# Kernel tuning notes

Hardware: AMD Instinct MI355X
Metric: run time of the kernel (lower is better)

The kernel has to match this reference:

```python
import jax, jax.numpy as jnp
import numpy as np

NPOINT = 2048
RADII = (0.4, 0.8)
NSAMPLES = (16, 32)
EPS = 1e-5


def _fps(xyz, npoint):
    # iterative farthest point sampling, start at index 0 (matches CUDA kernel)
    B, N, _ = xyz.shape

    def step(carry, _):
        dist, last = carry  # dist [B,N], last [B]
        lx = jnp.take_along_axis(xyz, last[:, None, None], axis=1)  # [B,1,3]
        d = jnp.sum((xyz - lx) ** 2, axis=-1)  # [B,N]
        dist = jnp.minimum(dist, d)
        nxt = jnp.argmax(dist, axis=1).astype(jnp.int32)
        return (dist, nxt), last

    init = (jnp.full((B, N), 1e10, xyz.dtype), jnp.zeros((B,), jnp.int32))
    _, idxs = jax.lax.scan(step, init, None, length=npoint)
    return idxs.T  # [B, npoint]


def _ball_query(radius, nsample, xyz, new_xyz):
    # first-nsample points within radius, in original order; pad with first hit (0 if none)
    N = xyz.shape[1]
    d2 = jnp.sum((new_xyz[:, :, None, :] - xyz[:, None, :, :]) ** 2, axis=-1)  # [B,S,N]
    mask = d2 < radius * radius
    ar = jnp.arange(N, dtype=jnp.int32)
    key = jnp.where(mask, ar, N + ar)  # in-range first, stable original order
    order = jnp.argsort(key, axis=-1)[..., :nsample].astype(jnp.int32)  # [B,S,ns]
    cnt = mask.sum(axis=-1, keepdims=True)  # [B,S,1]
    valid = jnp.arange(nsample) < cnt
    return jnp.where(valid, order, order[..., :1])


def _bn_relu(x):
    # training-mode BatchNorm (gamma=1, beta=0) over all dims but channel (last)
    red = tuple(range(x.ndim - 1))
    mu = x.mean(axis=red, keepdims=True)
    var = x.var(axis=red, keepdims=True)
    return jax.nn.relu((x - mu) * jax.lax.rsqrt(var + EPS))


def _scale(xyz, new_xyz, feats, radius, nsample, ws):
    idx = _ball_query(radius, nsample, xyz, new_xyz)  # [B,S,ns]
    B, S, ns = idx.shape
    flat = idx.reshape(B, S * ns)
    gx = jnp.take_along_axis(xyz, flat[..., None], axis=1).reshape(B, S, ns, 3)
    gx = gx - new_xyz[:, :, None, :]  # relative coords
    gf = jnp.take_along_axis(feats, flat[..., None], axis=1).reshape(B, S, ns, -1)
    h = jnp.concatenate([gx, gf], axis=-1)  # [B,S,ns,3+C]
    for w in ws:
        h = _bn_relu(h @ w)  # pointwise conv (kernel 1) + BN + ReLU
    return h.max(axis=2)  # max-pool over group -> [B,S,Cout]


def setup_inputs() -> dict:
    key = jax.random.key(0)
    ks = jax.random.split(key, 16)
    s = 0.02
    return {
        "xyz": jax.random.normal(ks[0], (8, 8192, 3), jnp.float32),
        "features": jax.random.normal(ks[1], (8, 8192, 64), jnp.float32),
        "w0_0": jax.random.normal(ks[2], (67, 64), jnp.float32) * s,
        "w0_1": jax.random.normal(ks[3], (64, 64), jnp.float32) * s,
        "w0_2": jax.random.normal(ks[4], (64, 128), jnp.float32) * s,
        "w1_0": jax.random.normal(ks[5], (67, 64), jnp.float32) * s,
        "w1_1": jax.random.normal(ks[6], (64, 64), jnp.float32) * s,
        "w1_2": jax.random.normal(ks[7], (64, 128), jnp.float32) * s,
        "agg_w": jax.random.normal(ks[8], (256, 256), jnp.float32) * s,
        "agg_b": jax.random.normal(ks[9], (256,), jnp.float32) * s,
        "conf_w": jax.random.normal(ks[10], (256, 256), jnp.float32) * s,
        "cls_w": jax.random.normal(ks[11], (256, 3), jnp.float32) * s,
        "cls_b": jax.random.normal(ks[12], (3,), jnp.float32) * s,
    }


def reference(xyz, features, w0_0, w0_1, w0_2, w1_0, w1_1, w1_2,
              agg_w, agg_b, conf_w, cls_w, cls_b):
    idx = _fps(xyz, NPOINT)  # [B,S]
    new_xyz = jnp.take_along_axis(xyz, idx[..., None], axis=1)  # [B,S,3]
    f0 = _scale(xyz, new_xyz, features, RADII[0], NSAMPLES[0], (w0_0, w0_1, w0_2))
    f1 = _scale(xyz, new_xyz, features, RADII[1], NSAMPLES[1], (w1_0, w1_1, w1_2))
    h = jnp.concatenate([f0, f1], axis=-1)  # [B,S,256]
    h = _bn_relu(h @ agg_w + agg_b)  # aggregation Linear + BN + ReLU
    c = _bn_relu(h @ conf_w)  # confidence hidden layer
    cls = c @ cls_w + cls_b  # [B,S,num_class]
    return new_xyz, h, cls
```

## Files before the change

### kernel.cpp

```cpp
#include <hip/hip_runtime.h>
#include <cstdint>
#include <cstddef>

constexpr int Bb = 8;
constexpr int Nn = 8192;
constexpr int Ss = 2048;
constexpr int BS = Bb * Ss;
constexpr int NSL = 32;

typedef float vfloat2 __attribute__((ext_vector_type(2)));

__global__ __launch_bounds__(1024) void fps_kernel(const float* __restrict__ xyz,
                                                   float* __restrict__ new_xyz) {
  __shared__ float lx[Nn * 3];
  __shared__ int sidx[Ss];
  __shared__ unsigned long long slotV[2];
  __shared__ int slotI[2];
  const int b = blockIdx.x;
  const int tid = threadIdx.x;
  const float* xb = xyz + (size_t)b * Nn * 3;
  for (int e = tid; e < Nn * 3; e += 1024) lx[e] = xb[e];
  if (tid == 0) {
    slotV[0] = 0ull; slotV[1] = 0ull;
    slotI[0] = 0x7fffffff; slotI[1] = 0x7fffffff;
  }
  __syncthreads();

  vfloat2 px2[4], py2[4], pz2[4], df2[4];
  double dist[8];
#pragma unroll
  for (int jj = 0; jj < 4; ++jj) {
    const int p0 = tid + (2 * jj) * 1024, p1 = tid + (2 * jj + 1) * 1024;
    px2[jj] = (vfloat2){lx[p0 * 3 + 0], lx[p1 * 3 + 0]};
    py2[jj] = (vfloat2){lx[p0 * 3 + 1], lx[p1 * 3 + 1]};
    pz2[jj] = (vfloat2){lx[p0 * 3 + 2], lx[p1 * 3 + 2]};
    df2[jj] = (vfloat2){3.0e38f, 3.0e38f};
    dist[2 * jj] = 1e10;
    dist[2 * jj + 1] = 1e10;
  }
  float lmax = 3.0e38f;
  int cur = 0;
  double lv = -1.0;
  int li = 0x7fffffff;
  float lv32 = -1.0f;
  float wv32_c = -1.0f;
  for (int i = 0; i < Ss; ++i) {
    if (tid == 0) sidx[i] = cur;
    const float cxf = lx[cur * 3 + 0], cyf = lx[cur * 3 + 1], czf = lx[cur * 3 + 2];
    const vfloat2 cx2 = {cxf, cxf}, cy2 = {cyf, cyf}, cz2 = {czf, czf};
    const bool wasTop = (lv32 == wv32_c);
    vfloat2 d2v[4];
#pragma unroll
    for (int jj = 0; jj < 4; ++jj) {
      const vfloat2 dx = px2[jj] - cx2;
      const vfloat2 dy = py2[jj] - cy2;
      const vfloat2 dz = pz2[jj] - cz2;
      d2v[jj] = dx * dx + dy * dy + dz * dz;
    }
    const float dmin = fminf(fminf(fminf(d2v[0].x, d2v[0].y), fminf(d2v[1].x, d2v[1].y)),
                             fminf(fminf(d2v[2].x, d2v[2].y), fminf(d2v[3].x, d2v[3].y)));
    bool changed = false;
    if (dmin <= lmax) {
#pragma unroll
      for (int j = 0; j < 8; ++j) {
        const float d2s = d2v[j >> 1][j & 1];
        const float dfs = (j & 1) ? df2[j >> 1].y : df2[j >> 1].x;
        if (d2s <= dfs) {
          const float pxs = px2[j >> 1][j & 1];
          const float pys = py2[j >> 1][j & 1];
          const float pzs = pz2[j >> 1][j & 1];
          double dx = __dsub_rn((double)pxs, (double)cxf);
          double dy = __dsub_rn((double)pys, (double)cyf);
          double dz = __dsub_rn((double)pzs, (double)czf);
          double d = __dadd_rn(__dadd_rn(__dmul_rn(dx, dx), __dmul_rn(dy, dy)),
                               __dmul_rn(dz, dz));
          if (d < dist[j]) {
            dist[j] = d;
            const float dfn = (float)d * 1.000002f;
            if (j & 1) df2[j >> 1].y = dfn; else df2[j >> 1].x = dfn;
            changed = true;
          }
        }
      }
      if (changed) {
        lv = -1.0;
        li = 0;
#pragma unroll
        for (int j = 0; j < 8; ++j) {
          if (dist[j] > lv) { lv = dist[j]; li = tid + j * 1024; }
        }
        lv32 = (float)lv;
        lmax = fmaxf(fmaxf(fmaxf(df2[0].x, df2[0].y), fmaxf(df2[1].x, df2[1].y)),
                     fmaxf(fmaxf(df2[2].x, df2[2].y), fmaxf(df2[3].x, df2[3].y)));
      }
    }
    const unsigned long long topChanged = __ballot(changed && wasTop);
    if (topChanged) {
      float m32 = lv32;
#pragma unroll
      for (int off = 1; off < 64; off <<= 1) m32 = fmaxf(m32, __shfl_xor(m32, off));
      wv32_c = m32;
    }
    const int pb = i & 1;
    if (lv32 == wv32_c) atomicMax(&slotV[pb], (unsigned long long)__double_as_longlong(lv));
    __syncthreads();
    const double W = __longlong_as_double((long long)slotV[pb]);
    if (lv == W) atomicMin(&slotI[pb], li);
    if (tid == 0) {
      slotV[pb ^ 1] = 0ull;
      slotI[pb ^ 1] = 0x7fffffff;
    }
    __syncthreads();
    cur = slotI[pb];
  }
  __syncthreads();
  float* nxb = new_xyz + (size_t)b * Ss * 3;
  for (int e = tid; e < Ss * 3; e += 1024) {
    const int i = e / 3, c = e - i * 3;
    nxb[e] = lx[sidx[i] * 3 + c];
  }
}

__global__ __launch_bounds__(256) void ballq_kernel(const float* __restrict__ xyz,
                                                    const float* __restrict__ nxyz,
                                                    int* __restrict__ idx0,
                                                    int* __restrict__ idx1) {
  const int wid = threadIdx.x >> 6, lane = threadIdx.x & 63;
  const int bs = blockIdx.x * 4 + wid;
  const int b = bs >> 11;
  const float* xb = xyz + (size_t)b * Nn * 3;
  const float cxf = nxyz[bs * 3 + 0];
  const float cyf = nxyz[bs * 3 + 1];
  const float czf = nxyz[bs * 3 + 2];
  const double R0d = 0.4 * 0.4, R1d = 0.8 * 0.8;
  const float R0lo = 0.16f * (1.0f - 1e-5f), R0hi = 0.16f * (1.0f + 1e-5f);
  const float R1lo = 0.64f * (1.0f - 1e-5f), R1hi = 0.64f * (1.0f + 1e-5f);
  int cnt0 = 0, cnt1 = 0, first0 = 0, first1 = 0;
  const unsigned long long lmask = (1ull << lane) - 1ull;
  for (int base = 0; base < Nn; base += 64) {
    const int p = base + lane;
    const float pxs = xb[p * 3 + 0], pys = xb[p * 3 + 1], pzs = xb[p * 3 + 2];
    const float dxf = pxs - cxf, dyf = pys - cyf, dzf = pzs - czf;
    const float d2f = fmaf(dxf, dxf, fmaf(dyf, dyf, dzf * dzf));
    bool in0, in1;
    if (d2f < R0lo) in0 = true;
    else if (d2f > R0hi) in0 = false;
    else {
      double dx = __dsub_rn((double)pxs, (double)cxf);
      double dy = __dsub_rn((double)pys, (double)cyf);
      double dz = __dsub_rn((double)pzs, (double)czf);
      double d2 = __dadd_rn(__dadd_rn(__dmul_rn(dx, dx), __dmul_rn(dy, dy)), __dmul_rn(dz, dz));
      in0 = d2 < R0d;
    }
    if (d2f < R1lo) in1 = true;
    else if (d2f > R1hi) in1 = false;
    else {
      double dx = __dsub_rn((double)pxs, (double)cxf);
      double dy = __dsub_rn((double)pys, (double)cyf);
      double dz = __dsub_rn((double)pzs, (double)czf);
      double d2 = __dadd_rn(__dadd_rn(__dmul_rn(dx, dx), __dmul_rn(dy, dy)), __dmul_rn(dz, dz));
      in1 = d2 < R1d;
    }
    unsigned long long m0 = __ballot(in0);
    unsigned long long m1 = __ballot(in1);
    if (cnt0 < 16 && m0) {
      if (cnt0 == 0) first0 = base + __builtin_ctzll(m0);
      int r = (int)__popcll(m0 & lmask);
      if (in0 && cnt0 + r < 16) idx0[bs * 16 + cnt0 + r] = p;
      cnt0 += (int)__popcll(m0);
    }
    if (cnt1 < 32 && m1) {
      if (cnt1 == 0) first1 = base + __builtin_ctzll(m1);
      int r = (int)__popcll(m1 & lmask);
      if (in1 && cnt1 + r < 32) idx1[bs * 32 + cnt1 + r] = p;
      cnt1 += (int)__popcll(m1);
    }
    if (cnt0 >= 16 && cnt1 >= 32) break;
  }
  const int f0 = cnt0 < 16 ? cnt0 : 16;
  for (int j = f0 + lane; j < 16; j += 64) idx0[bs * 16 + j] = first0;
  const int f1 = cnt1 < 32 ? cnt1 : 32;
  for (int j = f1 + lane; j < 32; j += 64) idx1[bs * 32 + j] = first1;
}

template <int COUT, int KTOT, int MODE, int NS, bool POOL, bool BIAS>
__global__ __launch_bounds__(256) void mlp_gemm(
    const float* __restrict__ xin, const float* __restrict__ xin2,
    const float* __restrict__ stIn, const float* __restrict__ stIn2,
    float invM1, float invM2,
    const float* __restrict__ w, const float* __restrict__ bias,
    const int* __restrict__ gidx, const float* __restrict__ xyz,
    const float* __restrict__ nxyz, const float* __restrict__ feats,
    float* __restrict__ hw, float* __restrict__ out, float* __restrict__ Sout) {
  constexpr int KC = (KTOT <= 68) ? KTOT : 32;
  constexpr int KCP = (KC + 3) & ~3;
  constexpr int NCH = (KTOT + KC - 1) / KC;
  constexpr int TC = COUT / 16;
  constexpr int TC2 = TC / 2;
  constexpr int XPAD = (KCP % 32 == 0) ? KCP + 4 : KCP;
  constexpr int XSZ = 64 * XPAD;
  constexpr int EPI = (POOL ? 48 : 32) * COUT;
  constexpr int SM = (XSZ + KCP * COUT > EPI) ? (XSZ + KCP * COUT) : EPI;
  constexpr int BNSZ = (MODE == 0) ? 0 : 512;
  __shared__ __align__(16) float smem[SM + BNSZ];
  __shared__ int rowP[(MODE == 0) ? 64 : 1];
  __shared__ float rowC[(MODE == 0) ? 192 : 1];
  float* xS = smem;
  float* wS = smem + XSZ;
  float* bnM = smem + SM;
  float* bnR = smem + SM + 256;

  const int tid = threadIdx.x;
  const int cg = tid & 15, rg = tid >> 4;
  const int row0 = blockIdx.x * 64;

  if constexpr (MODE == 0) {
    if (tid < 64) {
      const int rowg = row0 + tid;
      const int bs = rowg / NS;
      const int bb = bs >> 11;
      rowP[tid] = bb * Nn + gidx[rowg];
      rowC[tid * 3 + 0] = nxyz[bs * 3 + 0];
      rowC[tid * 3 + 1] = nxyz[bs * 3 + 1];
      rowC[tid * 3 + 2] = nxyz[bs * 3 + 2];
    }
    __syncthreads();
  } else {
    for (int c = tid; c < KTOT; c += 256) {
      float sum = 0.f, sq = 0.f, im;
      if constexpr (MODE == 2) {
        const float* base = (c < 128) ? stIn : stIn2;
        const int cc = (c < 128) ? c : c - 128;
        im = (c < 128) ? invM1 : invM2;
#pragma unroll
        for (int s = 0; s < NSL; ++s) {
          sum += base[cc * NSL + s];
          sq += base[(128 + cc) * NSL + s];
        }
      } else {
        constexpr int C = (MODE == 1) ? 64 : 256;
        im = invM1;
#pragma unroll
        for (int s = 0; s < NSL; ++s) {
          sum += stIn[c * NSL + s];
          sq += stIn[(C + c) * NSL + s];
        }
      }
      const float mu = sum * im;
      const float var = sq * im - mu * mu;
      bnM[c] = mu;
      bnR[c] = 1.0f / sqrtf(var + 1e-5f);
    }
    __syncthreads();
  }

  vfloat2 acc2[4][TC2];
#pragma unroll
  for (int i = 0; i < 4; ++i)
#pragma unroll
    for (int t = 0; t < TC2; ++t) acc2[i][t] = (vfloat2){0.f, 0.f};

  for (int ch = 0; ch < NCH; ++ch) {
    const int k0 = ch * KC;
    if (ch) __syncthreads();
    for (int e = tid; e < 64 * KCP; e += 256) {
      const int r = e / KCP, kk = e - r * KCP;
      const int kg = k0 + kk;
      const int rowg = row0 + r;
      float v;
      if (kg >= KTOT) {
        v = 0.f;
      } else if constexpr (MODE == 0) {
        if (kg < 3)
          v = xyz[rowP[r] * 3 + kg] - rowC[r * 3 + kg];
        else
          v = feats[(rowP[r] << 6) + (kg - 3)];
      } else if constexpr (MODE == 1) {
        v = fmaxf((xin[(size_t)rowg * 64 + kg] - bnM[kg]) * bnR[kg], 0.f);
      } else if constexpr (MODE == 2) {
        if (kg < 128)
          v = fmaxf((xin[(size_t)rowg * 128 + kg] - bnM[kg]) * bnR[kg], 0.f);
        else
          v = fmaxf((xin2[(size_t)rowg * 128 + (kg - 128)] - bnM[kg]) * bnR[kg], 0.f);
      } else {
        v = fmaxf((xin[(size_t)rowg * 256 + kg] - bnM[kg]) * bnR[kg], 0.f);
        hw[(size_t)rowg * 256 + kg] = v;
      }
      xS[r * XPAD + kk] = v;
    }
    for (int e = tid; e < KCP * COUT; e += 256) {
      const int kk = e / COUT, c = e - kk * COUT;
      wS[kk * COUT + c] = (k0 + kk < KTOT) ? w[(size_t)(k0 + kk) * COUT + c] : 0.f;
    }
    __syncthreads();
    for (int kb = 0; kb < KCP; kb += 4) {
      float4 xv[4];
#pragma unroll
      for (int i = 0; i < 4; ++i)
        xv[i] = *(const float4*)&xS[(rg * 4 + i) * XPAD + kb];
#pragma unroll
      for (int t2 = 0; t2 < TC2; t2 += 2) {
        float4 wv0 = *(const float4*)&wS[(kb + 0) * COUT + cg * TC + 2 * t2];
        float4 wv1 = *(const float4*)&wS[(kb + 1) * COUT + cg * TC + 2 * t2];
        float4 wv2 = *(const float4*)&wS[(kb + 2) * COUT + cg * TC + 2 * t2];
        float4 wv3 = *(const float4*)&wS[(kb + 3) * COUT + cg * TC + 2 * t2];
#pragma unroll
        for (int i = 0; i < 4; ++i) {
          {
            const vfloat2 x2 = {xv[i].x, xv[i].x};
            acc2[i][t2]     += x2 * (vfloat2){wv0.x, wv0.y};
            acc2[i][t2 + 1] += x2 * (vfloat2){wv0.z, wv0.w};
          }
          {
            const vfloat2 x2 = {xv[i].y, xv[i].y};
            acc2[i][t2]     += x2 * (vfloat2){wv1.x, wv1.y};
            acc2[i][t2 + 1] += x2 * (vfloat2){wv1.z, wv1.w};
          }
          {
            const vfloat2 x2 = {xv[i].z, xv[i].z};
            acc2[i][t2]     += x2 * (vfloat2){wv2.x, wv2.y};
            acc2[i][t2 + 1] += x2 * (vfloat2){wv2.z, wv2.w};
          }
          {
            const vfloat2 x2 = {xv[i].w, xv[i].w};
            acc2[i][t2]     += x2 * (vfloat2){wv3.x, wv3.y};
            acc2[i][t2 + 1] += x2 * (vfloat2){wv3.z, wv3.w};
          }
        }
      }
    }
  }
  __syncthreads();
  if constexpr (BIAS) {
#pragma unroll
    for (int t = 0; t < TC; ++t) {
      const float bv = bias[cg * TC + t];
#pragma unroll
      for (int i = 0; i < 4; ++i) {
        if (t & 1) acc2[i][t >> 1].y += bv; else acc2[i][t >> 1].x += bv;
      }
    }
  }
  float* ssum = smem;
  float* ssq = smem + 16 * COUT;
  float* pbuf = smem + 32 * COUT;
  const int colb = cg * TC;
#pragma unroll
  for (int t = 0; t < TC; ++t) {
    float s = 0.f, q = 0.f, m = -3.4e38f;
#pragma unroll
    for (int i = 0; i < 4; ++i) {
      const float v = (t & 1) ? acc2[i][t >> 1].y : acc2[i][t >> 1].x;
      s += v;
      q = fmaf(v, v, q);
      m = fmaxf(m, v);
    }
    ssum[rg * COUT + colb + t] = s;
    ssq[rg * COUT + colb + t] = q;
    if constexpr (POOL) pbuf[rg * COUT + colb + t] = m;
  }
  __syncthreads();
  const int slot = blockIdx.x & (NSL - 1);
  for (int c = tid; c < COUT; c += 256) {
    float s = 0.f, q = 0.f;
#pragma unroll
    for (int rr = 0; rr < 16; ++rr) {
      s += ssum[rr * COUT + c];
      q += ssq[rr * COUT + c];
    }
    atomicAdd(&Sout[c * NSL + slot], s);
    atomicAdd(&Sout[(COUT + c) * NSL + slot], q);
  }
  if constexpr (POOL) {
    constexpr int G = 64 / NS, RPG = NS / 4;
    for (int o = tid; o < G * COUT; o += 256) {
      const int g = o / COUT, c = o - g * COUT;
      float m = pbuf[(g * RPG) * COUT + c];
#pragma unroll
      for (int qq = 1; qq < RPG; ++qq) m = fmaxf(m, pbuf[(g * RPG + qq) * COUT + c]);
      out[(size_t)(blockIdx.x * G + g) * COUT + c] = m;
    }
  } else {
#pragma unroll
    for (int i = 0; i < 4; ++i) {
      float* op = out + (size_t)(row0 + rg * 4 + i) * COUT + colb;
#pragma unroll
      for (int t2 = 0; t2 < TC2; t2 += 2) {
        *(float4*)(op + 2 * t2) = make_float4(acc2[i][t2].x, acc2[i][t2].y,
                                              acc2[i][t2 + 1].x, acc2[i][t2 + 1].y);
      }
    }
  }
}

__global__ __launch_bounds__(256) void cls_kernel(const float* __restrict__ craw,
                                                  const float* __restrict__ st,
                                                  const float* __restrict__ clsw,
                                                  const float* __restrict__ clsb,
                                                  float* __restrict__ outc) {
  __shared__ float bnM[256], bnR[256];
  const int tid = threadIdx.x;
  {
    float sum = 0.f, sq = 0.f;
#pragma unroll
    for (int s = 0; s < NSL; ++s) {
      sum += st[tid * NSL + s];
      sq += st[(256 + tid) * NSL + s];
    }
    const float im = 1.0f / 16384.0f;
    const float mu = sum * im;
    const float var = sq * im - mu * mu;
    bnM[tid] = mu;
    bnR[tid] = 1.0f / sqrtf(var + 1e-5f);
  }
  __syncthreads();
  const int wid = tid >> 6, lane = tid & 63;
  const int row = blockIdx.x * 4 + wid;
  const float* cr = craw + (size_t)row * 256;
  float a0 = 0.f, a1 = 0.f, a2 = 0.f;
#pragma unroll 4
  for (int k = lane; k < 256; k += 64) {
    float x = fmaxf((cr[k] - bnM[k]) * bnR[k], 0.f);
    a0 = fmaf(x, clsw[k * 3 + 0], a0);
    a1 = fmaf(x, clsw[k * 3 + 1], a1);
    a2 = fmaf(x, clsw[k * 3 + 2], a2);
  }
#pragma unroll
  for (int off = 32; off; off >>= 1) {
    a0 += __shfl_down(a0, off);
    a1 += __shfl_down(a1, off);
    a2 += __shfl_down(a2, off);
  }
  if (lane == 0) {
    outc[row * 3 + 0] = a0 + clsb[0];
    outc[row * 3 + 1] = a1 + clsb[1];
    outc[row * 3 + 2] = a2 + clsb[2];
  }
}

extern "C" void kernel_launch(void* const* d_in, const int* in_sizes, int n_in,
                              void* d_out, int out_size, void* d_ws, size_t ws_size,
                              hipStream_t stream) {
  (void)in_sizes; (void)n_in; (void)out_size; (void)ws_size;
  const float* xyz = (const float*)d_in[0];
  const float* feats = (const float*)d_in[1];
  const float* w00 = (const float*)d_in[2];
  const float* w01 = (const float*)d_in[3];
  const float* w02 = (const float*)d_in[4];
  const float* w10 = (const float*)d_in[5];
  const float* w11 = (const float*)d_in[6];
  const float* w12 = (const float*)d_in[7];
  const float* aggw = (const float*)d_in[8];
  const float* aggb = (const float*)d_in[9];
  const float* confw = (const float*)d_in[10];
  const float* clsw = (const float*)d_in[11];
  const float* clsb = (const float*)d_in[12];

  float* outp = (float*)d_out;
  float* nxyz = outp;
  float* hout = outp + (size_t)BS * 3;
  float* clsout = hout + (size_t)BS * 256;

  char* ws = (char*)d_ws;
  const size_t MB = 1u << 20;
  int* idx0 = (int*)(ws + 0);
  int* idx1 = (int*)(ws + 1 * MB);
  float* st = (float*)(ws + 3 * MB);
  float* pool0 = (float*)(ws + 12 * MB);
  float* pool1 = (float*)(ws + 20 * MB);
  float* aggraw = (float*)(ws + 28 * MB);
  float* confraw = (float*)(ws + 44 * MB);
  float* hA = (float*)(ws + 60 * MB);

  hipMemsetAsync(st, 0, 65536 * sizeof(float), stream);

  const float iM0 = 1.0f / 262144.0f;
  const float iM1 = 1.0f / 524288.0f;
  const float iMh = 1.0f / 16384.0f;

  fps_kernel<<<Bb, 1024, 0, stream>>>(xyz, nxyz);
  ballq_kernel<<<BS / 4, 256, 0, stream>>>(xyz, nxyz, idx0, idx1);

  mlp_gemm<64, 67, 0, 16, false, false><<<4096, 256, 0, stream>>>(
      nullptr, nullptr, nullptr, nullptr, 0.f, 0.f, w00, nullptr,
      idx0, xyz, nxyz, feats, nullptr, hA, st + 0);
  mlp_gemm<64, 64, 1, 1, false, false><<<4096, 256, 0, stream>>>(
      hA, nullptr, st + 0, nullptr, iM0, 0.f, w01, nullptr,
      nullptr, nullptr, nullptr, nullptr, nullptr, hA, st + 4096);
  mlp_gemm<128, 64, 1, 16, true, false><<<4096, 256, 0, stream>>>(
      hA, nullptr, st + 4096, nullptr, iM0, 0.f, w02, nullptr,
      nullptr, nullptr, nullptr, nullptr, nullptr, pool0, st + 8192);

  mlp_gemm<64, 67, 0, 32, false, false><<<8192, 256, 0, stream>>>(
      nullptr, nullptr, nullptr, nullptr, 0.f, 0.f, w10, nullptr,
      idx1, xyz, nxyz, feats, nullptr, hA, st + 16384);
  mlp_gemm<64, 64, 1, 1, false, false><<<8192, 256, 0, stream>>>(
      hA, nullptr, st + 16384, nullptr, iM1, 0.f, w11, nullptr,
      nullptr, nullptr, nullptr, nullptr, nullptr, hA, st + 20480);
  mlp_gemm<128, 64, 1, 32, true, false><<<8192, 256, 0, stream>>>(
      hA, nullptr, st + 20480, nullptr, iM1, 0.f, w12, nullptr,
      nullptr, nullptr, nullptr, nullptr, nullptr, pool1, st + 24576);

  mlp_gemm<256, 256, 2, 1, false, true><<<256, 256, 0, stream>>>(
      pool0, pool1, st + 8192, st + 24576, iM0, iM1, aggw, aggb,
      nullptr, nullptr, nullptr, nullptr, nullptr, aggraw, st + 32768);

  mlp_gemm<256, 256, 4, 1, false, false><<<256, 256, 0, stream>>>(
      aggraw, nullptr, st + 32768, nullptr, iMh, 0.f, confw, nullptr,
      nullptr, nullptr, nullptr, nullptr, hout, confraw, st + 49152);

  cls_kernel<<<BS / 4, 256, 0, stream>>>(confraw, st + 49152, clsw, clsb, clsout);
}
```

Measured before the change: 3.671 ms.

## Overlap FPS with ball query and first MLP layer in a persistent mega-kernel

Merges farthest point sampling, ball query and the first pointwise layer of both scales into one persistent kernel. Eight blocks run FPS and publish progress every 64 centers. The remaining blocks take work from atomic ticket queues, spin on the progress and flag counters, then run ball query and the gathered first GEMM as soon as their inputs are ready. This hides the mostly serial FPS latency behind the downstream work. The cost is spin-waiting, a dependence on all blocks being co-resident, and a workspace-size check that falls back to the old path when the workspace is too small.

Measured after the change: 3.702 ms. No clear change (+0.8%).

```diff
diff --git a/kernel.cpp b/kernel.cpp
--- a/kernel.cpp
+++ b/kernel.cpp
@@ -10,123 +10,21 @@
 
 typedef float vfloat2 __attribute__((ext_vector_type(2)));
 
-__global__ __launch_bounds__(1024) void fps_kernel(const float* __restrict__ xyz,
-                                                   float* __restrict__ new_xyz) {
-  __shared__ float lx[Nn * 3];
-  __shared__ int sidx[Ss];
-  __shared__ unsigned long long slotV[2];
-  __shared__ int slotI[2];
-  const int b = blockIdx.x;
-  const int tid = threadIdx.x;
-  const float* xb = xyz + (size_t)b * Nn * 3;
-  for (int e = tid; e < Nn * 3; e += 1024) lx[e] = xb[e];
-  if (tid == 0) {
-    slotV[0] = 0ull; slotV[1] = 0ull;
-    slotI[0] = 0x7fffffff; slotI[1] = 0x7fffffff;
-  }
-  __syncthreads();
-
-  vfloat2 px2[4], py2[4], pz2[4], df2[4];
-  double dist[8];
-#pragma unroll
-  for (int jj = 0; jj < 4; ++jj) {
-    const int p0 = tid + (2 * jj) * 1024, p1 = tid + (2 * jj + 1) * 1024;
-    px2[jj] = (vfloat2){lx[p0 * 3 + 0], lx[p1 * 3 + 0]};
-    py2[jj] = (vfloat2){lx[p0 * 3 + 1], lx[p1 * 3 + 1]};
-    pz2[jj] = (vfloat2){lx[p0 * 3 + 2], lx[p1 * 3 + 2]};
-    df2[jj] = (vfloat2){3.0e38f, 3.0e38f};
-    dist[2 * jj] = 1e10;
-    dist[2 * jj + 1] = 1e10;
-  }
-  float lmax = 3.0e38f;
-  int cur = 0;
-  double lv = -1.0;
-  int li = 0x7fffffff;
-  float lv32 = -1.0f;
-  float wv32_c = -1.0f;
-  for (int i = 0; i < Ss; ++i) {
-    if (tid == 0) sidx[i] = cur;
-    const float cxf = lx[cur * 3 + 0], cyf = lx[cur * 3 + 1], czf = lx[cur * 3 + 2];
-    const vfloat2 cx2 = {cxf, cxf}, cy2 = {cyf, cyf}, cz2 = {czf, czf};
-    const bool wasTop = (lv32 == wv32_c);
-    vfloat2 d2v[4];
-#pragma unroll
-    for (int jj = 0; jj < 4; ++jj) {
-      const vfloat2 dx = px2[jj] - cx2;
-      const vfloat2 dy = py2[jj] - cy2;
-      const vfloat2 dz = pz2[jj] - cz2;
-      d2v[jj] = dx * dx + dy * dy + dz * dz;
-    }
-    const float dmin = fminf(fminf(fminf(d2v[0].x, d2v[0].y), fminf(d2v[1].x, d2v[1].y)),
-                             fminf(fminf(d2v[2].x, d2v[2].y), fminf(d2v[3].x, d2v[3].y)));
-    bool changed = false;
-    if (dmin <= lmax) {
-#pragma unroll
-      for (int j = 0; j < 8; ++j) {
-        const float d2s = d2v[j >> 1][j & 1];
-        const float dfs = (j & 1) ? df2[j >> 1].y : df2[j >> 1].x;
-        if (d2s <= dfs) {
-          const float pxs = px2[j >> 1][j & 1];
-          const float pys = py2[j >> 1][j & 1];
-          const float pzs = pz2[j >> 1][j & 1];
-          double dx = __dsub_rn((double)pxs, (double)cxf);
-          double dy = __dsub_rn((double)pys, (double)cyf);
-          double dz = __dsub_rn((double)pzs, (double)czf);
-          double d = __dadd_rn(__dadd_rn(__dmul_rn(dx, dx), __dmul_rn(dy, dy)),
-                               __dmul_rn(dz, dz));
-          if (d < dist[j]) {
-            dist[j] = d;
-            const float dfn = (float)d * 1.000002f;
-            if (j & 1) df2[j >> 1].y = dfn; else df2[j >> 1].x = dfn;
-            changed = true;
-          }
-        }
-      }
-      if (changed) {
-        lv = -1.0;
-        li = 0;
-#pragma unroll
-        for (int j = 0; j < 8; ++j) {
-          if (dist[j] > lv) { lv = dist[j]; li = tid + j * 1024; }
-        }
-        lv32 = (float)lv;
-        lmax = fmaxf(fmaxf(fmaxf(df2[0].x, df2[0].y), fmaxf(df2[1].x, df2[1].y)),
-                     fmaxf(fmaxf(df2[2].x, df2[2].y), fmaxf(df2[3].x, df2[3].y)));
-      }
-    }
-    const unsigned long long topChanged = __ballot(changed && wasTop);
-    if (topChanged) {
-      float m32 = lv32;
-#pragma unroll
-      for (int off = 1; off < 64; off <<= 1) m32 = fmaxf(m32, __shfl_xor(m32, off));
-      wv32_c = m32;
-    }
-    const int pb = i & 1;
-    if (lv32 == wv32_c) atomicMax(&slotV[pb], (unsigned long long)__double_as_longlong(lv));
-    __syncthreads();
-    const double W = __longlong_as_double((long long)slotV[pb]);
-    if (lv == W) atomicMin(&slotI[pb], li);
-    if (tid == 0) {
-      slotV[pb ^ 1] = 0ull;
-      slotI[pb ^ 1] = 0x7fffffff;
-    }
-    __syncthreads();
-    cur = slotI[pb];
-  }
-  __syncthreads();
-  float* nxb = new_xyz + (size_t)b * Ss * 3;
-  for (int e = tid; e < Ss * 3; e += 1024) {
-    const int i = e / 3, c = e - i * 3;
-    nxb[e] = lx[sidx[i] * 3 + c];
-  }
-}
-
-__global__ __launch_bounds__(256) void ballq_kernel(const float* __restrict__ xyz,
-                                                    const float* __restrict__ nxyz,
-                                                    int* __restrict__ idx0,
-                                                    int* __restrict__ idx1) {
-  const int wid = threadIdx.x >> 6, lane = threadIdx.x & 63;
-  const int bs = blockIdx.x * 4 + wid;
+struct Ctl {
+  int prog[8];
+  int pad0[24];
+  unsigned role; int padr[31];
+  unsigned tq0; int p1[31];
+  unsigned tq1; int p2[31];
+  unsigned tq2; int p3[31];
+  int flag[1024];
+};
+
+__device__ __forceinline__ void ballq_center(const int bs, const int lane,
+                                             const float* __restrict__ xyz,
+                                             const float* __restrict__ nxyz,
+                                             int* __restrict__ idx0,
+                                             int* __restrict__ idx1) {
   const int b = bs >> 11;
   const float* xb = xyz + (size_t)b * Nn * 3;
   const float cxf = nxyz[bs * 3 + 0];
@@ -181,6 +79,296 @@
   for (int j = f0 + lane; j < 16; j += 64) idx0[bs * 16 + j] = first0;
   const int f1 = cnt1 < 32 ? cnt1 : 32;
   for (int j = f1 + lane; j < 32; j += 64) idx1[bs * 32 + j] = first1;
+}
+
+__global__ __launch_bounds__(1024) void mega_kernel(
+    const float* __restrict__ xyz, const float* __restrict__ feats,
+    const float* __restrict__ w00, const float* __restrict__ w10,
+    float* __restrict__ new_xyz, int* __restrict__ idx0, int* __restrict__ idx1,
+    float* __restrict__ hA0, float* __restrict__ hA1,
+    float* __restrict__ st0, float* __restrict__ st1, Ctl* ctl) {
+  __shared__ __align__(16) unsigned char SM[107008];
+  __shared__ int sRole;
+  const int tid = threadIdx.x;
+
+  if (tid == 0)
+    sRole = (int)__hip_atomic_fetch_add(&ctl->role, 1u, __ATOMIC_RELAXED,
+                                        __HIP_MEMORY_SCOPE_AGENT);
+  __syncthreads();
+  const int role = sRole;
+
+  if (role < 8) {
+    float* lx = (float*)SM;
+    int* sidx = (int*)(SM + 98304);
+    unsigned long long* slotV = (unsigned long long*)(SM + 106496);
+    int* slotI = (int*)(SM + 106512);
+    const int b = role;
+    const float* xb = xyz + (size_t)b * Nn * 3;
+    float* nxb = new_xyz + (size_t)b * Ss * 3;
+    for (int e = tid; e < Nn * 3; e += 1024) lx[e] = xb[e];
+    if (tid == 0) {
+      slotV[0] = 0ull; slotV[1] = 0ull;
+      slotI[0] = 0x7fffffff; slotI[1] = 0x7fffffff;
+    }
+    __syncthreads();
+
+    vfloat2 px2[4], py2[4], pz2[4], df2[4];
+    double dist[8];
+#pragma unroll
+    for (int jj = 0; jj < 4; ++jj) {
+      const int p0 = tid + (2 * jj) * 1024, p1 = tid + (2 * jj + 1) * 1024;
+      px2[jj] = (vfloat2){lx[p0 * 3 + 0], lx[p1 * 3 + 0]};
+      py2[jj] = (vfloat2){lx[p0 * 3 + 1], lx[p1 * 3 + 1]};
+      pz2[jj] = (vfloat2){lx[p0 * 3 + 2], lx[p1 * 3 + 2]};
+      df2[jj] = (vfloat2){3.0e38f, 3.0e38f};
+      dist[2 * jj] = 1e10;
+      dist[2 * jj + 1] = 1e10;
+    }
+    float lmax = 3.0e38f;
+    int cur = 0;
+    double lv = -1.0;
+    int li = 0x7fffffff;
+    float lv32 = -1.0f;
+    float wv32_c = -1.0f;
+    for (int i = 0; i < Ss; ++i) {
+      if (tid == 0) sidx[i] = cur;
+      const float cxf = lx[cur * 3 + 0], cyf = lx[cur * 3 + 1], czf = lx[cur * 3 + 2];
+      const vfloat2 cx2 = {cxf, cxf}, cy2 = {cyf, cyf}, cz2 = {czf, czf};
+      const bool wasTop = (lv32 == wv32_c);
+      vfloat2 d2v[4];
+#pragma unroll
+      for (int jj = 0; jj < 4; ++jj) {
+        const vfloat2 dx = px2[jj] - cx2;
+        const vfloat2 dy = py2[jj] - cy2;
+        const vfloat2 dz = pz2[jj] - cz2;
+        d2v[jj] = dx * dx + dy * dy + dz * dz;
+      }
+      const float dmin = fminf(fminf(fminf(d2v[0].x, d2v[0].y), fminf(d2v[1].x, d2v[1].y)),
+                               fminf(fminf(d2v[2].x, d2v[2].y), fminf(d2v[3].x, d2v[3].y)));
+      bool changed = false;
+      if (dmin <= lmax) {
+#pragma unroll
+        for (int j = 0; j < 8; ++j) {
+          const float d2s = d2v[j >> 1][j & 1];
+          const float dfs = (j & 1) ? df2[j >> 1].y : df2[j >> 1].x;
+          if (d2s <= dfs) {
+            const float pxs = px2[j >> 1][j & 1];
+            const float pys = py2[j >> 1][j & 1];
+            const float pzs = pz2[j >> 1][j & 1];
+            double dx = __dsub_rn((double)pxs, (double)cxf);
+            double dy = __dsub_rn((double)pys, (double)cyf);
+            double dz = __dsub_rn((double)pzs, (double)czf);
+            double d = __dadd_rn(__dadd_rn(__dmul_rn(dx, dx), __dmul_rn(dy, dy)),
+                                 __dmul_rn(dz, dz));
+            if (d < dist[j]) {
+              dist[j] = d;
+              const float dfn = (float)d * 1.000002f;
+              if (j & 1) df2[j >> 1].y = dfn; else df2[j >> 1].x = dfn;
+              changed = true;
+            }
+          }
+        }
+        if (changed) {
+          lv = -1.0;
+          li = 0;
+#pragma unroll
+          for (int j = 0; j < 8; ++j) {
+            if (dist[j] > lv) { lv = dist[j]; li = tid + j * 1024; }
+          }
+          lv32 = (float)lv;
+          lmax = fmaxf(fmaxf(fmaxf(df2[0].x, df2[0].y), fmaxf(df2[1].x, df2[1].y)),
+                       fmaxf(fmaxf(df2[2].x, df2[2].y), fmaxf(df2[3].x, df2[3].y)));
+        }
+      }
+      const unsigned long long topChanged = __ballot(changed && wasTop);
+      if (topChanged) {
+        float m32 = lv32;
+#pragma unroll
+        for (int off = 1; off < 64; off <<= 1) m32 = fmaxf(m32, __shfl_xor(m32, off));
+        wv32_c = m32;
+      }
+      const int pb = i & 1;
+      if (lv32 == wv32_c) atomicMax(&slotV[pb], (unsigned long long)__double_as_longlong(lv));
+      __syncthreads();
+      const double W = __longlong_as_double((long long)slotV[pb]);
+      if (lv == W) atomicMin(&slotI[pb], li);
+      if (tid == 0) {
+        slotV[pb ^ 1] = 0ull;
+        slotI[pb ^ 1] = 0x7fffffff;
+      }
+      __syncthreads();
+      cur = slotI[pb];
+      if ((i & 63) == 63) {
+        const int base = i - 63;
+        for (int e = tid; e < 192; e += 1024) {
+          const int ci = base + e / 3, c = e - (e / 3) * 3;
+          nxb[ci * 3 + c] = lx[sidx[ci] * 3 + c];
+        }
+        __threadfence();
+        __syncthreads();
+        if (tid == 0)
+          __hip_atomic_store(&ctl->prog[b], i + 1, __ATOMIC_RELEASE, __HIP_MEMORY_SCOPE_AGENT);
+      }
+    }
+    return;
+  }
+
+  float* wS = (float*)SM;
+  float* xSall = (float*)(SM + 17408);
+  int* rowPall = (int*)(SM + 87040);
+  float* rowCall = (float*)(SM + 88064);
+  int* sTick = (int*)(SM + 91136);
+  const int vtid = tid & 255, sub = tid >> 8;
+  const int cg = vtid & 15, rg = vtid >> 4;
+  float* xS = xSall + sub * (64 * 68);
+  int* rP = rowPall + sub * 64;
+  float* rC = rowCall + sub * 192;
+  const int wid = tid >> 6, lane = tid & 63;
+
+  for (;;) {
+    __syncthreads();
+    if (tid == 0) *sTick = (int)atomicAdd(&ctl->tq0, 1u);
+    __syncthreads();
+    const int t = *sTick;
+    if (t >= 1024) break;
+    const int b = t & 7, gL = t >> 3;
+    if (tid == 0) {
+      while (__hip_atomic_load(&ctl->prog[b], __ATOMIC_RELAXED, __HIP_MEMORY_SCOPE_AGENT) <
+             gL * 16 + 16)
+        __builtin_amdgcn_s_sleep(8);
+    }
+    __syncthreads();
+    (void)__hip_atomic_load(&ctl->prog[b], __ATOMIC_ACQUIRE, __HIP_MEMORY_SCOPE_AGENT);
+    ballq_center(b * 2048 + gL * 16 + wid, lane, xyz, new_xyz, idx0, idx1);
+    __threadfence();
+    __syncthreads();
+    if (tid == 0)
+      __hip_atomic_store(&ctl->flag[t], 1, __ATOMIC_RELEASE, __HIP_MEMORY_SCOPE_AGENT);
+  }
+
+  for (int phase = 0; phase < 2; ++phase) {
+    const float* wsrc = phase ? w10 : w00;
+    const int* gidx = phase ? idx1 : idx0;
+    float* Sout = phase ? st1 : st0;
+    float* out = phase ? hA1 : hA0;
+    const int log2ns = phase ? 5 : 4;
+    const int NT = phase ? 2048 : 1024;
+    unsigned* tq = phase ? &ctl->tq2 : &ctl->tq1;
+    __syncthreads();
+    for (int e = tid; e < 68 * 64; e += 1024) {
+      const int kk = e >> 6, c = e & 63;
+      wS[e] = (kk < 67) ? wsrc[kk * 64 + c] : 0.f;
+    }
+    for (;;) {
+      __syncthreads();
+      if (tid == 0) *sTick = (int)atomicAdd(tq, 1u);
+      __syncthreads();
+      const int v = *sTick;
+      if (v >= NT) break;
+      const int b = v & 7, j = v >> 3;
+      const int u = (phase ? b * 256 : b * 128) + j;
+      const int fIdx = ((phase ? (j >> 1) : j) << 3) | b;
+      if (tid == 0) {
+        while (!__hip_atomic_load(&ctl->flag[fIdx], __ATOMIC_RELAXED, __HIP_MEMORY_SCOPE_AGENT))
+          __builtin_amdgcn_s_sleep(8);
+      }
+      __syncthreads();
+      (void)__hip_atomic_load(&ctl->flag[fIdx], __ATOMIC_ACQUIRE, __HIP_MEMORY_SCOPE_AGENT);
+      const int g = 4 * u + sub;
+      const int row0 = g * 64;
+      if (vtid < 64) {
+        const int rowg = row0 + vtid;
+        const int bs = rowg >> log2ns;
+        const int bb = bs >> 11;
+        rP[vtid] = (bb << 13) + gidx[rowg];
+        rC[vtid * 3 + 0] = new_xyz[bs * 3 + 0];
+        rC[vtid * 3 + 1] = new_xyz[bs * 3 + 1];
+        rC[vtid * 3 + 2] = new_xyz[bs * 3 + 2];
+      }
+      __syncthreads();
+      for (int e = vtid; e < 64 * 68; e += 256) {
+        const int r = e / 68, kk = e - r * 68;
+        float val;
+        if (kk >= 67) val = 0.f;
+        else if (kk < 3) val = xyz[rP[r] * 3 + kk] - rC[r * 3 + kk];
+        else val = feats[(rP[r] << 6) + (kk - 3)];
+        xS[r * 68 + kk] = val;
+      }
+      __syncthreads();
+      vfloat2 acc2[4][2];
+#pragma unroll
+      for (int i = 0; i < 4; ++i) {
+        acc2[i][0] = (vfloat2){0.f, 0.f};
+        acc2[i][1] = (vfloat2){0.f, 0.f};
+      }
+      for (int kb = 0; kb < 68; kb += 4) {
+        float4 xv[4];
+#pragma unroll
+        for (int i = 0; i < 4; ++i)
+          xv[i] = *(const float4*)&xS[(rg * 4 + i) * 68 + kb];
+        const float4 wv0 = *(const float4*)&wS[(kb + 0) * 64 + cg * 4];
+        const float4 wv1 = *(const float4*)&wS[(kb + 1) * 64 + cg * 4];
+        const float4 wv2 = *(const float4*)&wS[(kb + 2) * 64 + cg * 4];
+        const float4 wv3 = *(const float4*)&wS[(kb + 3) * 64 + cg * 4];
+#pragma unroll
+        for (int i = 0; i < 4; ++i) {
+          { const vfloat2 x2 = {xv[i].x, xv[i].x};
+            acc2[i][0] += x2 * (vfloat2){wv0.x, wv0.y};
+            acc2[i][1] += x2 * (vfloat2){wv0.z, wv0.w}; }
+          { const vfloat2 x2 = {xv[i].y, xv[i].y};
+            acc2[i][0] += x2 * (vfloat2){wv1.x, wv1.y};
+            acc2[i][1] += x2 * (vfloat2){wv1.z, wv1.w}; }
+          { const vfloat2 x2 = {xv[i].z, xv[i].z};
+            acc2[i][0] += x2 * (vfloat2){wv2.x, wv2.y};
+            acc2[i][1] += x2 * (vfloat2){wv2.z, wv2.w}; }
+          { const vfloat2 x2 = {xv[i].w, xv[i].w};
+            acc2[i][0] += x2 * (vfloat2){wv3.x, wv3.y};
+            acc2[i][1] += x2 * (vfloat2){wv3.z, wv3.w}; }
+        }
+      }
+      __syncthreads();
+      float* ssum = xS;
+      float* ssq = xS + 1024;
+      const int colb = cg * 4;
+#pragma unroll
+      for (int t = 0; t < 4; ++t) {
+        float s = 0.f, q = 0.f;
+#pragma unroll
+        for (int i = 0; i < 4; ++i) {
+          const float val = (t & 1) ? acc2[i][t >> 1].y : acc2[i][t >> 1].x;
+          s += val;
+          q = fmaf(val, val, q);
+        }
+        ssum[rg * 64 + colb + t] = s;
+        ssq[rg * 64 + colb + t] = q;
+      }
+      __syncthreads();
+      const int slot = g & 31;
+      for (int c = vtid; c < 64; c += 256) {
+        float s = 0.f, q = 0.f;
+#pragma unroll
+        for (int rr = 0; rr < 16; ++rr) {
+          s += ssum[rr * 64 + c];
+          q += ssq[rr * 64 + c];
+        }
+        atomicAdd(&Sout[c * NSL + slot], s);
+        atomicAdd(&Sout[(64 + c) * NSL + slot], q);
+      }
+#pragma unroll
+      for (int i = 0; i < 4; ++i) {
+        float* op = out + (size_t)(row0 + rg * 4 + i) * 64 + colb;
+        *(float4*)op = make_float4(acc2[i][0].x, acc2[i][0].y, acc2[i][1].x, acc2[i][1].y);
+      }
+    }
+  }
+}
+
+__global__ __launch_bounds__(256) void ballq_kernel(const float* __restrict__ xyz,
+                                                    const float* __restrict__ nxyz,
+                                                    int* __restrict__ idx0,
+                                                    int* __restrict__ idx1) {
+  const int wid = threadIdx.x >> 6, lane = threadIdx.x & 63;
+  ballq_center(blockIdx.x * 4 + wid, lane, xyz, nxyz, idx0, idx1);
 }
 
 template <int COUT, int KTOT, int MODE, int NS, bool POOL, bool BIAS>
@@ -441,7 +629,7 @@
 extern "C" void kernel_launch(void* const* d_in, const int* in_sizes, int n_in,
                               void* d_out, int out_size, void* d_ws, size_t ws_size,
                               hipStream_t stream) {
-  (void)in_sizes; (void)n_in; (void)out_size; (void)ws_size;
+  (void)in_sizes; (void)n_in; (void)out_size;
   const float* xyz = (const float*)d_in[0];
   const float* feats = (const float*)d_in[1];
   const float* w00 = (const float*)d_in[2];
@@ -462,43 +650,67 @@
   float* clsout = hout + (size_t)BS * 256;
 
   char* ws = (char*)d_ws;
-  const size_t MB = 1u << 20;
+  const size_t MB = 1ull << 20;
   int* idx0 = (int*)(ws + 0);
   int* idx1 = (int*)(ws + 1 * MB);
-  float* st = (float*)(ws + 3 * MB);
-  float* pool0 = (float*)(ws + 12 * MB);
-  float* pool1 = (float*)(ws + 20 * MB);
-  float* aggraw = (float*)(ws + 28 * MB);
-  float* confraw = (float*)(ws + 44 * MB);
-  float* hA = (float*)(ws + 60 * MB);
+  Ctl* ctl = (Ctl*)(ws + 3 * MB + 512 * 1024);
+  const bool OV = ws_size >= 217ull * MB;
+
+  float *st, *pool0, *pool1, *aggraw, *confraw, *hA0, *hA1;
+  if (OV) {
+    st = (float*)(ws + 4 * MB);
+    pool0 = (float*)(ws + 5 * MB);
+    hA0 = (float*)(ws + 16 * MB);
+    hA1 = (float*)(ws + 83 * MB);
+    pool1 = (float*)(ws + 16 * MB);
+    aggraw = (float*)(ws + 24 * MB);
+    confraw = (float*)(ws + 40 * MB);
+  } else {
+    st = (float*)(ws + 3 * MB);
+    pool0 = (float*)(ws + 12 * MB);
+    pool1 = (float*)(ws + 20 * MB);
+    aggraw = (float*)(ws + 28 * MB);
+    confraw = (float*)(ws + 44 * MB);
+    hA0 = (float*)(ws + 60 * MB);
+    hA1 = hA0;
+  }
 
   hipMemsetAsync(st, 0, 65536 * sizeof(float), stream);
+  hipMemsetAsync(ctl, 0, sizeof(Ctl), stream);
 
   const float iM0 = 1.0f / 262144.0f;
   const float iM1 = 1.0f / 524288.0f;
   const float iMh = 1.0f / 16384.0f;
 
-  fps_kernel<<<Bb, 1024, 0, stream>>>(xyz, nxyz);
-  ballq_kernel<<<BS / 4, 256, 0, stream>>>(xyz, nxyz, idx0, idx1);
-
-  mlp_gemm<64, 67, 0, 16, false, false><<<4096, 256, 0, stream>>>(
-      nullptr, nullptr, nullptr, nullptr, 0.f, 0.f, w00, nullptr,
-      idx0, xyz, nxyz, feats, nullptr, hA, st + 0);
+  if (OV) {
+    mega_kernel<<<256, 1024, 0, stream>>>(xyz, feats, w00, w10, nxyz, idx0, idx1,
+                                          hA0, hA1, st + 0, st + 16384, ctl);
+  } else {
+    mega_kernel<<<8, 1024, 0, stream>>>(xyz, feats, w00, w10, nxyz, idx0, idx1,
+                                        hA0, hA1, st + 0, st + 16384, ctl);
+    ballq_kernel<<<BS / 4, 256, 0, stream>>>(xyz, nxyz, idx0, idx1);
+    mlp_gemm<64, 67, 0, 16, false, false><<<4096, 256, 0, stream>>>(
+        nullptr, nullptr, nullptr, nullptr, 0.f, 0.f, w00, nullptr,
+        idx0, xyz, nxyz, feats, nullptr, hA0, st + 0);
+  }
+
   mlp_gemm<64, 64, 1, 1, false, false><<<4096, 256, 0, stream>>>(
-      hA, nullptr, st + 0, nullptr, iM0, 0.f, w01, nullptr,
-      nullptr, nullptr, nullptr, nullptr, nullptr, hA, st + 4096);
+      hA0, nullptr, st + 0, nullptr, iM0, 0.f, w01, nullptr,
+      nullptr, nullptr, nullptr, nullptr, nullptr, hA0, st + 4096);
   mlp_gemm<128, 64, 1, 16, true, false><<<4096, 256, 0, stream>>>(
-      hA, nullptr, st + 4096, nullptr, iM0, 0.f, w02, nullptr,
+      hA0, nullptr, st + 4096, nullptr, iM0, 0.f, w02, nullptr,
       nullptr, nullptr, nullptr, nullptr, nullptr, pool0, st + 8192);
 
-  mlp_gemm<64, 67, 0, 32, false, false><<<8192, 256, 0, stream>>>(
-      nullptr, nullptr, nullptr, nullptr, 0.f, 0.f, w10, nullptr,
-      idx1, xyz, nxyz, feats, nullptr, hA, st + 16384);
+  if (!OV) {
+    mlp_gemm<64, 67, 0, 32, false, false><<<8192, 256, 0, stream>>>(
+        nullptr, nullptr, nullptr, nullptr, 0.f, 0.f, w10, nullptr,
+        idx1, xyz, nxyz, feats, nullptr, hA1, st + 16384);
+  }
   mlp_gemm<64, 64, 1, 1, false, false><<<8192, 256, 0, stream>>>(
-      hA, nullptr, st + 16384, nullptr, iM1, 0.f, w11, nullptr,
-      nullptr, nullptr, nullptr, nullptr, nullptr, hA, st + 20480);
+      hA1, nullptr, st + 16384, nullptr, iM1, 0.f, w11, nullptr,
+      nullptr, nullptr, nullptr, nullptr, nullptr, hA1, st + 20480);
   mlp_gemm<128, 64, 1, 32, true, false><<<8192, 256, 0, stream>>>(
-      hA, nullptr, st + 20480, nullptr, iM1, 0.f, w12, nullptr,
+      hA1, nullptr, st + 20480, nullptr, iM1, 0.f, w12, nullptr,
       nullptr, nullptr, nullptr, nullptr, nullptr, pool1, st + 24576);
 
   mlp_gemm<256, 256, 2, 1, false, true><<<256, 256, 0, stream>>>(
```

## Merge both scales' MLP layers into single launches with split block ranges

Applied to the files above, without the earlier changes.

Runs the two radius scales' MLP layers in one launch per layer. Block indices below a split point handle scale 0 and the rest handle scale 1, and each scale gets its own activation buffer so both can be in flight together. This cuts six launches to three and avoids the tail of the smaller scale-0 grids. The workspace layout changes, and the merged path is used only when the workspace is at least 217 MB; otherwise the old sequential launches run.

Result: no change. 3.626 ms (-1.2%).

```diff
diff --git a/kernel.cpp b/kernel.cpp
--- a/kernel.cpp
+++ b/kernel.cpp
@@ -183,7 +183,7 @@
   for (int j = f1 + lane; j < 32; j += 64) idx1[bs * 32 + j] = first1;
 }
 
-template <int COUT, int KTOT, int MODE, int NS, bool POOL, bool BIAS>
+template <int COUT, int KTOT, int MODE, int NS, bool POOL, bool BIAS, bool MERGED>
 __global__ __launch_bounds__(256) void mlp_gemm(
     const float* __restrict__ xin, const float* __restrict__ xin2,
     const float* __restrict__ stIn, const float* __restrict__ stIn2,
@@ -191,7 +191,11 @@
     const float* __restrict__ w, const float* __restrict__ bias,
     const int* __restrict__ gidx, const float* __restrict__ xyz,
     const float* __restrict__ nxyz, const float* __restrict__ feats,
-    float* __restrict__ hw, float* __restrict__ out, float* __restrict__ Sout) {
+    float* __restrict__ hw, float* __restrict__ out, float* __restrict__ Sout,
+    int split, int l2nsA, int l2nsB,
+    const float* __restrict__ xinB, const float* __restrict__ stInB, float invMB,
+    const float* __restrict__ wB, const int* __restrict__ gidxB,
+    float* __restrict__ outB, float* __restrict__ SoutB) {
   constexpr int KC = (KTOT <= 68) ? KTOT : 32;
   constexpr int KCP = (KC + 3) & ~3;
   constexpr int NCH = (KTOT + KC - 1) / KC;
@@ -212,14 +216,31 @@
 
   const int tid = threadIdx.x;
   const int cg = tid & 15, rg = tid >> 4;
-  const int row0 = blockIdx.x * 64;
+
+  int bid = blockIdx.x;
+  const float* xinP = xin;
+  const float* stP = stIn;
+  float invMP = invM1;
+  const float* wP = w;
+  const int* gidxP = gidx;
+  float* outP = out;
+  float* SoutP = Sout;
+  int l2ns = l2nsA;
+  if constexpr (MERGED) {
+    if (blockIdx.x >= split) {
+      bid = blockIdx.x - split;
+      xinP = xinB; stP = stInB; invMP = invMB; wP = wB; gidxP = gidxB;
+      outP = outB; SoutP = SoutB; l2ns = l2nsB;
+    }
+  }
+  const int row0 = bid * 64;
 
   if constexpr (MODE == 0) {
     if (tid < 64) {
       const int rowg = row0 + tid;
-      const int bs = rowg / NS;
+      const int bs = MERGED ? (rowg >> l2ns) : (rowg / NS);
       const int bb = bs >> 11;
-      rowP[tid] = bb * Nn + gidx[rowg];
+      rowP[tid] = bb * Nn + gidxP[rowg];
       rowC[tid * 3 + 0] = nxyz[bs * 3 + 0];
       rowC[tid * 3 + 1] = nxyz[bs * 3 + 1];
       rowC[tid * 3 + 2] = nxyz[bs * 3 + 2];
@@ -239,11 +260,11 @@
         }
       } else {
         constexpr int C = (MODE == 1) ? 64 : 256;
-        im = invM1;
+        im = invMP;
 #pragma unroll
         for (int s = 0; s < NSL; ++s) {
-          sum += stIn[c * NSL + s];
-          sq += stIn[(C + c) * NSL + s];
+          sum += stP[c * NSL + s];
+          sq += stP[(C + c) * NSL + s];
         }
       }
       const float mu = sum * im;
@@ -276,21 +297,21 @@
         else
           v = feats[(rowP[r] << 6) + (kg - 3)];
       } else if constexpr (MODE == 1) {
-        v = fmaxf((xin[(size_t)rowg * 64 + kg] - bnM[kg]) * bnR[kg], 0.f);
+        v = fmaxf((xinP[(size_t)rowg * 64 + kg] - bnM[kg]) * bnR[kg], 0.f);
       } else if constexpr (MODE == 2) {
         if (kg < 128)
           v = fmaxf((xin[(size_t)rowg * 128 + kg] - bnM[kg]) * bnR[kg], 0.f);
         else
           v = fmaxf((xin2[(size_t)rowg * 128 + (kg - 128)] - bnM[kg]) * bnR[kg], 0.f);
       } else {
-        v = fmaxf((xin[(size_t)rowg * 256 + kg] - bnM[kg]) * bnR[kg], 0.f);
+        v = fmaxf((xinP[(size_t)rowg * 256 + kg] - bnM[kg]) * bnR[kg], 0.f);
         hw[(size_t)rowg * 256 + kg] = v;
       }
       xS[r * XPAD + kk] = v;
     }
     for (int e = tid; e < KCP * COUT; e += 256) {
       const int kk = e / COUT, c = e - kk * COUT;
-      wS[kk * COUT + c] = (k0 + kk < KTOT) ? w[(size_t)(k0 + kk) * COUT + c] : 0.f;
+      wS[kk * COUT + c] = (k0 + kk < KTOT) ? wP[(size_t)(k0 + kk) * COUT + c] : 0.f;
     }
     __syncthreads();
     for (int kb = 0; kb < KCP; kb += 4) {
@@ -360,7 +381,7 @@
     if constexpr (POOL) pbuf[rg * COUT + colb + t] = m;
   }
   __syncthreads();
-  const int slot = blockIdx.x & (NSL - 1);
+  const int slot = bid & (NSL - 1);
   for (int c = tid; c < COUT; c += 256) {
     float s = 0.f, q = 0.f;
 #pragma unroll
@@ -368,22 +389,23 @@
       s += ssum[rr * COUT + c];
       q += ssq[rr * COUT + c];
     }
-    atomicAdd(&Sout[c * NSL + slot], s);
-    atomicAdd(&Sout[(COUT + c) * NSL + slot], q);
+    atomicAdd(&SoutP[c * NSL + slot], s);
+    atomicAdd(&SoutP[(COUT + c) * NSL + slot], q);
   }
   if constexpr (POOL) {
-    constexpr int G = 64 / NS, RPG = NS / 4;
+    constexpr int Gc = 64 / NS, RPGc = NS / 4;
+    const int G = MERGED ? (64 >> l2ns) : Gc;
+    const int RPG = MERGED ? (1 << (l2ns - 2)) : RPGc;
     for (int o = tid; o < G * COUT; o += 256) {
       const int g = o / COUT, c = o - g * COUT;
       float m = pbuf[(g * RPG) * COUT + c];
-#pragma unroll
       for (int qq = 1; qq < RPG; ++qq) m = fmaxf(m, pbuf[(g * RPG + qq) * COUT + c]);
-      out[(size_t)(blockIdx.x * G + g) * COUT + c] = m;
+      outP[(size_t)(bid * G + g) * COUT + c] = m;
     }
   } else {
 #pragma unroll
     for (int i = 0; i < 4; ++i) {
-      float* op = out + (size_t)(row0 + rg * 4 + i) * COUT + colb;
+      float* op = outP + (size_t)(row0 + rg * 4 + i) * COUT + colb;
 #pragma unroll
       for (int t2 = 0; t2 < TC2; t2 += 2) {
         *(float4*)(op + 2 * t2) = make_float4(acc2[i][t2].x, acc2[i][t2].y,
@@ -438,10 +460,12 @@
   }
 }
 
+#define NOMERGE 0x40000000, 0, 0, nullptr, nullptr, 0.f, nullptr, nullptr, nullptr, nullptr
+
 extern "C" void kernel_launch(void* const* d_in, const int* in_sizes, int n_in,
                               void* d_out, int out_size, void* d_ws, size_t ws_size,
                               hipStream_t stream) {
-  (void)in_sizes; (void)n_in; (void)out_size; (void)ws_size;
+  (void)in_sizes; (void)n_in; (void)out_size;
   const float* xyz = (const float*)d_in[0];
   const float* feats = (const float*)d_in[1];
   const float* w00 = (const float*)d_in[2];
@@ -462,15 +486,29 @@
   float* clsout = hout + (size_t)BS * 256;
 
   char* ws = (char*)d_ws;
-  const size_t MB = 1u << 20;
+  const size_t MB = 1ull << 20;
   int* idx0 = (int*)(ws + 0);
   int* idx1 = (int*)(ws + 1 * MB);
-  float* st = (float*)(ws + 3 * MB);
-  float* pool0 = (float*)(ws + 12 * MB);
-  float* pool1 = (float*)(ws + 20 * MB);
-  float* aggraw = (float*)(ws + 28 * MB);
-  float* confraw = (float*)(ws + 44 * MB);
-  float* hA = (float*)(ws + 60 * MB);
+  const bool MG = ws_size >= 217ull * MB;
+
+  float *st, *pool0, *pool1, *aggraw, *confraw, *hA0, *hA1;
+  if (MG) {
+    st = (float*)(ws + 4 * MB);
+    pool0 = (float*)(ws + 5 * MB);
+    pool1 = (float*)(ws + 13 * MB);
+    hA0 = (float*)(ws + 24 * MB);
+    hA1 = (float*)(ws + 88 * MB);
+    aggraw = (float*)(ws + 24 * MB);
+    confraw = (float*)(ws + 40 * MB);
+  } else {
+    st = (float*)(ws + 3 * MB);
+    pool0 = (float*)(ws + 12 * MB);
+    pool1 = (float*)(ws + 20 * MB);
+    aggraw = (float*)(ws + 28 * MB);
+    confraw = (float*)(ws + 44 * MB);
+    hA0 = (float*)(ws + 60 * MB);
+    hA1 = hA0;
+  }
 
   hipMemsetAsync(st, 0, 65536 * sizeof(float), stream);
 
@@ -481,33 +519,47 @@
   fps_kernel<<<Bb, 1024, 0, stream>>>(xyz, nxyz);
   ballq_kernel<<<BS / 4, 256, 0, stream>>>(xyz, nxyz, idx0, idx1);
 
-  mlp_gemm<64, 67, 0, 16, false, false><<<4096, 256, 0, stream>>>(
-      nullptr, nullptr, nullptr, nullptr, 0.f, 0.f, w00, nullptr,
-      idx0, xyz, nxyz, feats, nullptr, hA, st + 0);
-  mlp_gemm<64, 64, 1, 1, false, false><<<4096, 256, 0, stream>>>(
-      hA, nullptr, st + 0, nullptr, iM0, 0.f, w01, nullptr,
-      nullptr, nullptr, nullptr, nullptr, nullptr, hA, st + 4096);
-  mlp_gemm<128, 64, 1, 16, true, false><<<4096, 256, 0, stream>>>(
-      hA, nullptr, st + 4096, nullptr, iM0, 0.f, w02, nullptr,
-      nullptr, nullptr, nullptr, nullptr, nullptr, pool0, st + 8192);
-
-  mlp_gemm<64, 67, 0, 32, false, false><<<8192, 256, 0, stream>>>(
-      nullptr, nullptr, nullptr, nullptr, 0.f, 0.f, w10, nullptr,
-      idx1, xyz, nxyz, feats, nullptr, hA, st + 16384);
-  mlp_gemm<64, 64, 1, 1, false, false><<<8192, 256, 0, stream>>>(
-      hA, nullptr, st + 16384, nullptr, iM1, 0.f, w11, nullptr,
-      nullptr, nullptr, nullptr, nullptr, nullptr, hA, st + 20480);
-  mlp_gemm<128, 64, 1, 32, true, false><<<8192, 256, 0, stream>>>(
-      hA, nullptr, st + 20480, nullptr, iM1, 0.f, w12, nullptr,
-      nullptr, nullptr, nullptr, nullptr, nullptr, pool1, st + 24576);
-
-  mlp_gemm<256, 256, 2, 1, false, true><<<256, 256, 0, stream>>>(
+  if (MG) {
+    mlp_gemm<64, 67, 0, 16, false, false, true><<<12288, 256, 0, stream>>>(
+        nullptr, nullptr, nullptr, nullptr, 0.f, 0.f, w00, nullptr,
+        idx0, xyz, nxyz, feats, nullptr, hA0, st + 0,
+        4096, 4, 5, nullptr, nullptr, 0.f, w10, idx1, hA1, st + 16384);
+    mlp_gemm<64, 64, 1, 1, false, false, true><<<12288, 256, 0, stream>>>(
+        hA0, nullptr, st + 0, nullptr, iM0, 0.f, w01, nullptr,
+        nullptr, nullptr, nullptr, nullptr, nullptr, hA0, st + 4096,
+        4096, 0, 0, hA1, st + 16384, iM1, w11, nullptr, hA1, st + 20480);
+    mlp_gemm<128, 64, 1, 16, true, false, true><<<12288, 256, 0, stream>>>(
+        hA0, nullptr, st + 4096, nullptr, iM0, 0.f, w02, nullptr,
+        nullptr, nullptr, nullptr, nullptr, nullptr, pool0, st + 8192,
+        4096, 4, 5, hA1, st + 20480, iM1, w12, nullptr, pool1, st + 24576);
+  } else {
+    mlp_gemm<64, 67, 0, 16, false, false, false><<<4096, 256, 0, stream>>>(
+        nullptr, nullptr, nullptr, nullptr, 0.f, 0.f, w00, nullptr,
+        idx0, xyz, nxyz, feats, nullptr, hA0, st + 0, NOMERGE);
+    mlp_gemm<64, 64, 1, 1, false, false, false><<<4096, 256, 0, stream>>>(
+        hA0, nullptr, st + 0, nullptr, iM0, 0.f, w01, nullptr,
+        nullptr, nullptr, nullptr, nullptr, nullptr, hA0, st + 4096, NOMERGE);
+    mlp_gemm<128, 64, 1, 16, true, false, false><<<4096, 256, 0, stream>>>(
+        hA0, nullptr, st + 4096, nullptr, iM0, 0.f, w02, nullptr,
+        nullptr, nullptr, nullptr, nullptr, nullptr, pool0, st + 8192, NOMERGE);
+    mlp_gemm<64, 67, 0, 32, false, false, false><<<8192, 256, 0, stream>>>(
+        nullptr, nullptr, nullptr, nullptr, 0.f, 0.f, w10, nullptr,
+        idx1, xyz, nxyz, feats, nullptr, hA1, st + 16384, NOMERGE);
+    mlp_gemm<64, 64, 1, 1, false, false, false><<<8192, 256, 0, stream>>>(
+        hA1, nullptr, st + 16384, nullptr, iM1, 0.f, w11, nullptr,
+        nullptr, nullptr, nullptr, nullptr, nullptr, hA1, st + 20480, NOMERGE);
+    mlp_gemm<128, 64, 1, 32, true, false, false><<<8192, 256, 0, stream>>>(
+        hA1, nullptr, st + 20480, nullptr, iM1, 0.f, w12, nullptr,
+        nullptr, nullptr, nullptr, nullptr, nullptr, pool1, st + 24576, NOMERGE);
+  }
+
+  mlp_gemm<256, 256, 2, 1, false, true, false><<<256, 256, 0, stream>>>(
       pool0, pool1, st + 8192, st + 24576, iM0, iM1, aggw, aggb,
-      nullptr, nullptr, nullptr, nullptr, nullptr, aggraw, st + 32768);
-
-  mlp_gemm<256, 256, 4, 1, false, false><<<256, 256, 0, stream>>>(
+      nullptr, nullptr, nullptr, nullptr, nullptr, aggraw, st + 32768, NOMERGE);
+
+  mlp_gemm<256, 256, 4, 1, false, false, false><<<256, 256, 0, stream>>>(
       aggraw, nullptr, st + 32768, nullptr, iMh, 0.f, confw, nullptr,
-      nullptr, nullptr, nullptr, nullptr, hout, confraw, st + 49152);
+      nullptr, nullptr, nullptr, nullptr, hout, confraw, st + 49152, NOMERGE);
 
   cls_kernel<<<BS / 4, 256, 0, stream>>>(confraw, st + 49152, clsw, clsb, clsout);
 }
```
